# Kernel tuning notes

Measured on AMD Instinct MI355X. Metric: run time of the kernel, lower is better.

The kernel has to match this reference:

```python
import jax, jax.numpy as jnp
import numpy as np

NSITES, NUP, BATCH = 128, 64, 4096


def _rand_distinct_sorted_idx(key, batch, nsites, nup):
    # per-sample distinct site indices (prefix of a random permutation), sorted
    u = jax.random.uniform(key, (batch, nsites))
    idx = jnp.argsort(u, axis=1)[:, :nup]
    return jnp.sort(idx, axis=1).astype(jnp.int32)


def setup_inputs() -> dict:
    key = jax.random.key(0)
    k1, k2, k3 = jax.random.split(key, 3)
    U = jax.random.normal(k1, (NSITES, NUP), dtype=jnp.float32)
    idx_up = _rand_distinct_sorted_idx(k2, BATCH, NSITES, NUP)
    idx_dn = _rand_distinct_sorted_idx(k3, BATCH, NSITES, NUP)
    return {"U": U, "idx_up": idx_up, "idx_dn": idx_dn}


def reference(U, idx_up, idx_dn):
    # psi(n) = det(n_up * U) * det(n_dn * U), returned in log form
    # gather rows per sample: (B, Nup, Nup)
    sign_up, logabs_up = jnp.linalg.slogdet(U[idx_up, :])
    sign_dn, logabs_dn = jnp.linalg.slogdet(U[idx_dn, :])
    # LogArray product: signs multiply, log-magnitudes add
    return (sign_up * sign_dn, logabs_up + logabs_dn)
```

## Files before the change

kernel.cpp:

```cpp
#include <hip/hip_runtime.h>

#define BATCH 4096
#define N 64

template<int CTRL>
__device__ __forceinline__ unsigned dpp_umax(unsigned x) {
    unsigned moved = (unsigned)__builtin_amdgcn_update_dpp(0, (int)x, CTRL, 0xf, 0xf, true);
    return (moved > x) ? moved : x;
}

__device__ __forceinline__ float lanebcastf(float v, int ps) {
    return __uint_as_float(__builtin_amdgcn_readlane(__float_as_uint(v), ps));
}

__device__ __forceinline__ int pivot_argmax(float col, bool alive, int lane) {
    unsigned t = (__float_as_uint(col) & 0x7FFFFFC0u) | (unsigned)lane;
    unsigned r = alive ? t : 0u;
    r = dpp_umax<0x111>(r);
    r = dpp_umax<0x112>(r);
    r = dpp_umax<0x114>(r);
    r = dpp_umax<0x118>(r);
    r = dpp_umax<0x142>(r);
    r = dpp_umax<0x143>(r);
    return (int)(((unsigned)__builtin_amdgcn_readlane((int)r, 63)) & 63u);
}

__global__ __launch_bounds__(64) void restricted_det_kernel(
    const float* __restrict__ U,
    const int* __restrict__ idx_up,
    const int* __restrict__ idx_dn,
    float* __restrict__ out)
{
    const int lane = threadIdx.x;
    const int wid  = blockIdx.x;

    const int site0 = idx_up[wid * N + lane];
    const int site1 = idx_dn[wid * N + lane];

    float l2sum = 0.0f;
    unsigned sbits = 0u;
    int inv = 0;

    #pragma unroll 1
    for (int spin = 0; spin < 2; ++spin) {
        const int site = (spin == 0) ? site0 : site1;

        float a[N];
        const float4* __restrict__ row = reinterpret_cast<const float4*>(U + (long)site * N);
        #pragma unroll
        for (int q = 0; q < N / 4; ++q) {
            float4 v = row[q];
            a[4*q+0]=v.x; a[4*q+1]=v.y; a[4*q+2]=v.z; a[4*q+3]=v.w;
        }

        unsigned long long chosen = 0ull;
        bool alive = true;

        int ps = pivot_argmax(a[0], alive, lane);

        #pragma unroll
        for (int k = 0; k < N - 1; ++k) {
            inv += __popcll(chosen >> ps);
            chosen |= (1ull << ps);
            alive = alive && (lane != ps);

            const float pv = lanebcastf(a[k], ps);
            sbits ^= __float_as_uint(pv) & 0x80000000u;
            l2sum += __log2f(__builtin_fabsf(pv));

            const float m = a[k] * __builtin_amdgcn_rcpf(pv);

            {
                const float uv = lanebcastf(a[k + 1], ps);
                a[k + 1] = __builtin_fmaf(-m, uv, a[k + 1]);
            }
            const int ps_next = pivot_argmax(a[k + 1], alive, lane);

            #pragma unroll
            for (int j = k + 2; j < N; ++j) {
                const float uv = lanebcastf(a[j], ps);
                a[j] = __builtin_fmaf(-m, uv, a[j]);
            }

            ps = ps_next;
        }

        inv += __popcll(chosen >> ps);
        chosen |= (1ull << ps);
        const float pv = lanebcastf(a[N - 1], ps);
        sbits ^= __float_as_uint(pv) & 0x80000000u;
        l2sum += __log2f(__builtin_fabsf(pv));
    }

    if (lane == 0) {
        const float sgn =
            (((sbits >> 31) ^ ((unsigned)inv & 1u)) != 0u) ? -1.0f : 1.0f;
        out[wid] = sgn;
        out[BATCH + wid] = l2sum * 0.69314718055994530942f;
    }
}

extern "C" void kernel_launch(void* const* d_in, const int* in_sizes, int n_in,
                              void* d_out, int out_size, void* d_ws, size_t ws_size,
                              hipStream_t stream) {
    const float* U      = (const float*)d_in[0];
    const int*   idx_up = (const int*)d_in[1];
    const int*   idx_dn = (const int*)d_in[2];
    float* out = (float*)d_out;

    dim3 block(64);
    dim3 grid(BATCH);
    hipLaunchKernelGGL(restricted_det_kernel, grid, block, 0, stream,
                       U, idx_up, idx_dn, out);
}
```

Before: 160.6 us.

## Restructure LU elimination into four fixed-width 16-step rolled blocks with ping-pong registers

```diff
diff --git a/kernel.cpp b/kernel.cpp
--- a/kernel.cpp
+++ b/kernel.cpp
@@ -25,6 +25,51 @@
     return (int)(((unsigned)__builtin_amdgcn_readlane((int)r, 63)) & 63u);
 }
 
+template<int W>
+__device__ __forceinline__ void lu_step(float (&src)[N], float (&dst)[N],
+                                        int &ps, bool &alive,
+                                        unsigned long long &chosen, int &inv,
+                                        unsigned &sbits, float &l2sum,
+                                        int lane)
+{
+    inv += __popcll(chosen >> ps);
+    chosen |= (1ull << ps);
+    alive = alive && (lane != ps);
+
+    const float pv = lanebcastf(src[0], ps);
+    sbits ^= __float_as_uint(pv) & 0x80000000u;
+    l2sum += __log2f(__builtin_fabsf(pv));
+
+    const float m = src[0] * __builtin_amdgcn_rcpf(pv);
+
+    {
+        const float uv = lanebcastf(src[1], ps);
+        dst[0] = __builtin_fmaf(-m, uv, src[1]);
+    }
+    const int ps_next = pivot_argmax(dst[0], alive, lane);
+
+    #pragma unroll
+    for (int j = 2; j <= W; ++j) {
+        const float uv = lanebcastf(src[j], ps);
+        dst[j - 1] = __builtin_fmaf(-m, uv, src[j]);
+    }
+    ps = ps_next;
+}
+
+template<int W>
+__device__ __forceinline__ void lu_block16(float (&a)[N], float (&b)[N],
+                                           int &ps, bool &alive,
+                                           unsigned long long &chosen, int &inv,
+                                           unsigned &sbits, float &l2sum,
+                                           int lane)
+{
+    #pragma unroll 1
+    for (int t = 0; t < 8; ++t) {
+        lu_step<W>(a, b, ps, alive, chosen, inv, sbits, l2sum, lane);
+        lu_step<W>(b, a, ps, alive, chosen, inv, sbits, l2sum, lane);
+    }
+}
+
 __global__ __launch_bounds__(64) void restricted_det_kernel(
     const float* __restrict__ U,
     const int* __restrict__ idx_up,
@@ -45,12 +90,15 @@
     for (int spin = 0; spin < 2; ++spin) {
         const int site = (spin == 0) ? site0 : site1;
 
-        float a[N];
-        const float4* __restrict__ row = reinterpret_cast<const float4*>(U + (long)site * N);
-        #pragma unroll
-        for (int q = 0; q < N / 4; ++q) {
-            float4 v = row[q];
-            a[4*q+0]=v.x; a[4*q+1]=v.y; a[4*q+2]=v.z; a[4*q+3]=v.w;
+        float a[N], b[N];
+        {
+            const float4* __restrict__ row =
+                reinterpret_cast<const float4*>(U + (long)site * N);
+            #pragma unroll
+            for (int q = 0; q < N / 4; ++q) {
+                float4 v = row[q];
+                a[4*q+0]=v.x; a[4*q+1]=v.y; a[4*q+2]=v.z; a[4*q+3]=v.w;
+            }
         }
 
         unsigned long long chosen = 0ull;
@@ -58,38 +106,10 @@
 
         int ps = pivot_argmax(a[0], alive, lane);
 
-        #pragma unroll
-        for (int k = 0; k < N - 1; ++k) {
-            inv += __popcll(chosen >> ps);
-            chosen |= (1ull << ps);
-            alive = alive && (lane != ps);
-
-            const float pv = lanebcastf(a[k], ps);
-            sbits ^= __float_as_uint(pv) & 0x80000000u;
-            l2sum += __log2f(__builtin_fabsf(pv));
-
-            const float m = a[k] * __builtin_amdgcn_rcpf(pv);
-
-            {
-                const float uv = lanebcastf(a[k + 1], ps);
-                a[k + 1] = __builtin_fmaf(-m, uv, a[k + 1]);
-            }
-            const int ps_next = pivot_argmax(a[k + 1], alive, lane);
-
-            #pragma unroll
-            for (int j = k + 2; j < N; ++j) {
-                const float uv = lanebcastf(a[j], ps);
-                a[j] = __builtin_fmaf(-m, uv, a[j]);
-            }
-
-            ps = ps_next;
-        }
-
-        inv += __popcll(chosen >> ps);
-        chosen |= (1ull << ps);
-        const float pv = lanebcastf(a[N - 1], ps);
-        sbits ^= __float_as_uint(pv) & 0x80000000u;
-        l2sum += __log2f(__builtin_fabsf(pv));
+        lu_block16<63>(a, b, ps, alive, chosen, inv, sbits, l2sum, lane);
+        lu_block16<47>(a, b, ps, alive, chosen, inv, sbits, l2sum, lane);
+        lu_block16<31>(a, b, ps, alive, chosen, inv, sbits, l2sum, lane);
+        lu_block16<15>(a, b, ps, alive, chosen, inv, sbits, l2sum, lane);
     }
 
     if (lane == 0) {
```

Measured after the change: 167.0 us. 1.04x slower.
